# Kernel tuning notes

Measured on AMD Instinct MI355X. Metric: run time of the kernel, lower is better.

Reference implementation:

```python
import jax, jax.numpy as jnp
import numpy as np

D_MODEL = 1024
NUM_HEADS = 16
BATCH = 2
SEQ = 2048


def setup_inputs() -> dict:
    key = jax.random.key(0)
    ks = jax.random.split(key, 5)
    scale = 1.0 / np.sqrt(D_MODEL)
    x = jax.random.normal(ks[0], (BATCH, SEQ, D_MODEL), dtype=jnp.float32)
    Wq = jax.random.normal(ks[1], (D_MODEL, D_MODEL), dtype=jnp.float32) * scale
    Wk = jax.random.normal(ks[2], (D_MODEL, D_MODEL), dtype=jnp.float32) * scale
    Wv = jax.random.normal(ks[3], (D_MODEL, D_MODEL), dtype=jnp.float32) * scale
    Wo = jax.random.normal(ks[4], (D_MODEL, D_MODEL), dtype=jnp.float32) * scale
    return {"x": x, "Wq": Wq, "Wk": Wk, "Wv": Wv, "Wo": Wo}


def reference(x, Wq, Wk, Wv, Wo):
    b, s, d_model = x.shape
    h = NUM_HEADS
    d_head = d_model // h
    # projections (Linear with weight [out,in]: y = x @ W^T)
    def split_heads(y):
        return y.reshape(b, s, h, d_head).transpose(0, 2, 1, 3)  # b h s d
    q = split_heads(x @ Wq.T)
    k = split_heads(x @ Wk.T)
    v = split_heads(x @ Wv.T)
    # full (non-flash) attention, as in the original
    att = jnp.einsum('bhsd,bhtd->bhst', q, k) / jnp.sqrt(jnp.float32(d_head)).astype(x.dtype)
    att = jax.nn.softmax(att, axis=-1)
    out = jnp.einsum('bhst,bhtd->bhsd', att, v)
    out = out.transpose(0, 2, 1, 3).reshape(b, s, d_model)
    return out @ Wo.T
```

## Files before the change

kernel.cpp:

```cpp
#include <hip/hip_runtime.h>
#include <stdint.h>

typedef __bf16 bf16_t;
typedef __bf16 bf16x4 __attribute__((ext_vector_type(4)));
typedef __bf16 bf16x8 __attribute__((ext_vector_type(8)));
typedef float  f32x4  __attribute__((ext_vector_type(4)));
typedef float  f32x16 __attribute__((ext_vector_type(16)));

#define D_MODEL 1024
#define SEQ     2048
#define BATCH   2
#define NHEAD   16
#define DHEAD   64
#define NROWS   (BATCH*SEQ)
#define LDT     72
#define LDA     72

__device__ __forceinline__ void async_ld16(const bf16_t* g, bf16_t* l) {
    __builtin_amdgcn_global_load_lds(
        (const __attribute__((address_space(1))) uint32_t*)(uintptr_t)g,
        (__attribute__((address_space(3))) uint32_t*)(uintptr_t)l,
        16, 0, 0);
}

__device__ __forceinline__ bf16x8 cvt8(f32x4 lo, f32x4 hi) {
    bf16x8 o;
#pragma unroll
    for (int i = 0; i < 4; ++i) { o[i] = (bf16_t)lo[i]; o[4 + i] = (bf16_t)hi[i]; }
    return o;
}

__global__ void __launch_bounds__(256)
k_cvt(const float* __restrict__ w0, const float* __restrict__ w1,
      const float* __restrict__ w2, const float* __restrict__ w3,
      const float* __restrict__ x,
      bf16_t* __restrict__ o0, bf16_t* __restrict__ o1,
      bf16_t* __restrict__ o2, bf16_t* __restrict__ o3,
      bf16_t* __restrict__ ox)
{
    const int blk = blockIdx.x;
    const float* s; bf16_t* d; int bi;
    if (blk < 2048) { s = x; d = ox; bi = blk; }
    else {
        const int t = blk - 2048, sel = t >> 9; bi = t & 511;
        s = (sel == 0) ? w0 : (sel == 1) ? w1 : (sel == 2) ? w2 : w3;
        d = (sel == 0) ? o0 : (sel == 1) ? o1 : (sel == 2) ? o2 : o3;
    }
    const size_t i = ((size_t)bi * 256 + threadIdx.x) * 8;
    *(bf16x8*)(d + i) = cvt8(*(const f32x4*)(s + i), *(const f32x4*)(s + i + 4));
}

template <int OUT_MODE>
__device__ __forceinline__ void gemm128(bf16_t* __restrict__ smem,
                                        const bf16_t* __restrict__ X,
                                        const bf16_t* __restrict__ W,
                                        void* __restrict__ Yv,
                                        int m0, int n0, float oscale)
{
    bf16_t* lA = smem;
    bf16_t* lB = smem + 128 * 32;

    const int tid  = threadIdx.x;
    const int lane = tid & 63;
    const int w    = tid >> 6;
    const int l15  = lane & 15;
    const int quad = lane >> 4;

    const int c0 = tid, c1 = tid + 256;
    const int r0 = c0 >> 2, r1 = c1 >> 2;
    const int kc0 = (c0 & 3) ^ ((r0 >> 1) & 3);
    const int kc1 = (c1 & 3) ^ ((r1 >> 1) & 3);
    const bf16_t* gA0 = X + (size_t)(m0 + r0) * D_MODEL + kc0 * 8;
    const bf16_t* gA1 = X + (size_t)(m0 + r1) * D_MODEL + kc1 * 8;
    const bf16_t* gB0 = W + (size_t)(n0 + r0) * D_MODEL + kc0 * 8;
    const bf16_t* gB1 = W + (size_t)(n0 + r1) * D_MODEL + kc1 * 8;

    int am[4], bn[4];
    const int mw = (w >> 1) * 64, nw = (w & 1) * 64;
#pragma unroll
    for (int i = 0; i < 4; ++i) {
        const int ra = mw + i * 16 + l15;
        am[i] = ra * 32 + (quad ^ ((ra >> 1) & 3)) * 8;
        const int rb = nw + i * 16 + l15;
        bn[i] = rb * 32 + (quad ^ ((rb >> 1) & 3)) * 8;
    }

    f32x4 acc[4][4];
#pragma unroll
    for (int i = 0; i < 4; ++i)
#pragma unroll
        for (int j = 0; j < 4; ++j) acc[i][j] = f32x4{0.f, 0.f, 0.f, 0.f};

    for (int k0 = 0; k0 < D_MODEL; k0 += 32) {
        __syncthreads();
        async_ld16(gA0 + k0, &lA[c0 * 8]);
        async_ld16(gA1 + k0, &lA[c1 * 8]);
        async_ld16(gB0 + k0, &lB[c0 * 8]);
        async_ld16(gB1 + k0, &lB[c1 * 8]);
        __syncthreads();

        bf16x8 af[4], bfr[4];
#pragma unroll
        for (int i = 0; i < 4; ++i) af[i]  = *(const bf16x8*)&lA[am[i]];
#pragma unroll
        for (int i = 0; i < 4; ++i) bfr[i] = *(const bf16x8*)&lB[bn[i]];
#pragma unroll
        for (int mi = 0; mi < 4; ++mi)
#pragma unroll
            for (int ni = 0; ni < 4; ++ni)
                acc[mi][ni] = __builtin_amdgcn_mfma_f32_16x16x32_bf16(
                    af[mi], bfr[ni], acc[mi][ni], 0, 0, 0);
    }

    if constexpr (OUT_MODE == 1) {
        bf16_t* lT = smem;
#pragma unroll
        for (int h0 = 0; h0 < 2; ++h0) {
            __syncthreads();
            if ((w >> 1) == h0) {
#pragma unroll
                for (int mi = 0; mi < 4; ++mi)
#pragma unroll
                    for (int ni = 0; ni < 4; ++ni) {
                        bf16x4 pk;
#pragma unroll
                        for (int r = 0; r < 4; ++r)
                            pk[r] = (bf16_t)(acc[mi][ni][r] * oscale);
                        const int col = nw + ni * 16 + l15;
                        *(bf16x4*)&lT[col * LDT + mi * 16 + quad * 4] = pk;
                    }
            }
            __syncthreads();
            const int col = tid & 127;
            const int seg = tid >> 7;
            const int brow = m0 + h0 * 64;
            const int b = brow >> 11, sb = brow & 2047;
            const int cg = n0 + col;
            bf16_t* dst = (bf16_t*)Yv +
                ((size_t)((b << 4) | (cg >> 6)) * 64 + (cg & 63)) * SEQ + sb;
#pragma unroll
            for (int u = 0; u < 4; ++u)
                *(bf16x8*)(dst + seg * 32 + u * 8) =
                    *(const bf16x8*)&lT[col * LDT + seg * 32 + u * 8];
        }
    } else {
#pragma unroll
        for (int mi = 0; mi < 4; ++mi)
#pragma unroll
            for (int ni = 0; ni < 4; ++ni)
#pragma unroll
                for (int r = 0; r < 4; ++r) {
                    const int row = m0 + mw + mi * 16 + quad * 4 + r;
                    const int col = n0 + nw + ni * 16 + l15;
                    const float vv = acc[mi][ni][r] * oscale;
                    if constexpr (OUT_MODE == 0)
                        ((bf16_t*)Yv)[(size_t)row * D_MODEL + col] = (bf16_t)vv;
                    else
                        ((float*)Yv)[(size_t)row * D_MODEL + col] = vv;
                }
    }
}

__global__ void __launch_bounds__(256)
k_gemm_qkv(const bf16_t* __restrict__ X,
           const bf16_t* __restrict__ Wq, const bf16_t* __restrict__ Wk,
           const bf16_t* __restrict__ Wv,
           bf16_t* __restrict__ Qb, bf16_t* __restrict__ Kb, bf16_t* __restrict__ Vt)
{
    __shared__ __align__(16) bf16_t smem[128 * LDT];
    const int sel = blockIdx.y >> 3;
    const int n0  = (blockIdx.y & 7) * 128;
    const int m0  = blockIdx.x * 128;
    if (sel == 0)      gemm128<0>(smem, X, Wq, Qb, m0, n0, 0.125f);
    else if (sel == 1) gemm128<0>(smem, X, Wk, Kb, m0, n0, 1.0f);
    else               gemm128<1>(smem, X, Wv, Vt, m0, n0, 1.0f);
}

__global__ void __launch_bounds__(256)
k_gemm_out(const bf16_t* __restrict__ X, const bf16_t* __restrict__ W,
           float* __restrict__ Y)
{
    __shared__ __align__(16) bf16_t smem[128 * LDT];
    gemm128<2>(smem, X, W, Y, blockIdx.x * 128, blockIdx.y * 128, 1.0f);
}

__global__ void __launch_bounds__(256, 4)
k_attn(const bf16_t* __restrict__ Qb, const bf16_t* __restrict__ Kb,
       const bf16_t* __restrict__ Vt, bf16_t* __restrict__ Ob)
{
    __shared__ __align__(16) bf16_t lK[64 * LDA];
    __shared__ __align__(16) bf16_t lV[64 * LDA];
    __shared__ __align__(16) bf16_t Pm[64 * LDA];

    const int tid  = threadIdx.x;
    const int lane = tid & 63;
    const int w    = tid >> 6;
    const int l31  = lane & 31;
    const int h    = lane >> 5;
    const int a    = w & 1;
    const int b    = w >> 1;

    const int bh = blockIdx.x;
    const int b_ = bh >> 4, hh = bh & 15;
    const int q0 = blockIdx.y * 64;

    const size_t base = (size_t)b_ * SEQ * D_MODEL + (size_t)hh * DHEAD;
    const bf16_t* Qp = Qb + base;
    const bf16_t* Kp = Kb + base;
    const bf16_t* Vp = Vt + (size_t)bh * DHEAD * SEQ;

    const int qrow = q0 + b * 32 + l31;
    bf16x8 qf[4];
#pragma unroll
    for (int c = 0; c < 4; ++c)
        qf[c] = *(const bf16x8*)&Qp[(size_t)qrow * D_MODEL + c * 16 + h * 8];

    const int c0 = tid, c1 = tid + 256;
    const int r0 = c0 >> 3, ch0 = c0 & 7;
    const int r1 = c1 >> 3, ch1 = c1 & 7;
    const bf16_t* gK0 = Kp + (size_t)r0 * D_MODEL + ch0 * 8;
    const bf16_t* gK1 = Kp + (size_t)r1 * D_MODEL + ch1 * 8;
    const bf16_t* gV0 = Vp + (size_t)r0 * SEQ + ch0 * 8;
    const bf16_t* gV1 = Vp + (size_t)r1 * SEQ + ch1 * 8;
    const int sK0 = r0 * LDA + ch0 * 8, sK1 = r1 * LDA + ch1 * 8;

    bf16x8 ones;
#pragma unroll
    for (int i = 0; i < 8; ++i) ones[i] = (bf16_t)1.0f;

    f32x16 acc_o, acc_l;
#pragma unroll
    for (int i = 0; i < 16; ++i) { acc_o[i] = 0.f; acc_l[i] = 0.f; }

    bf16x8 pk0 = *(const bf16x8*)gK0;
    bf16x8 pk1 = *(const bf16x8*)gK1;
    bf16x8 pv0 = *(const bf16x8*)gV0;
    bf16x8 pv1 = *(const bf16x8*)gV1;

    for (int kv0 = 0; kv0 < SEQ; kv0 += 64) {
        __syncthreads();
        *(bf16x8*)&lK[sK0] = pk0;
        *(bf16x8*)&lK[sK1] = pk1;
        *(bf16x8*)&lV[sK0] = pv0;
        *(bf16x8*)&lV[sK1] = pv1;
        __syncthreads();

        const int nkv = kv0 + 64;
        if (nkv < SEQ) {
            pk0 = *(const bf16x8*)(gK0 + (size_t)nkv * D_MODEL);
            pk1 = *(const bf16x8*)(gK1 + (size_t)nkv * D_MODEL);
            pv0 = *(const bf16x8*)(gV0 + nkv);
            pv1 = *(const bf16x8*)(gV1 + nkv);
        }

        f32x16 st;
#pragma unroll
        for (int i = 0; i < 16; ++i) st[i] = 0.f;
#pragma unroll
        for (int c = 0; c < 4; ++c) {
            bf16x8 kf = *(const bf16x8*)&lK[(a * 32 + l31) * LDA + c * 16 + h * 8];
            st = __builtin_amdgcn_mfma_f32_32x32x16_bf16(kf, qf[c], st, 0, 0, 0);
        }

#pragma unroll
        for (int g = 0; g < 4; ++g) {
            bf16x4 pp;
#pragma unroll
            for (int r = 0; r < 4; ++r) pp[r] = (bf16_t)__expf(st[g * 4 + r]);
            *(bf16x4*)&Pm[(b * 32 + l31) * LDA + a * 32 + g * 8 + h * 4] = pp;
        }
        __syncthreads();

#pragma unroll
        for (int c = 0; c < 4; ++c) {
            bf16x8 pf = *(const bf16x8*)&Pm[(b * 32 + l31) * LDA + c * 16 + h * 8];
            bf16x8 vf = *(const bf16x8*)&lV[(a * 32 + l31) * LDA + c * 16 + h * 8];
            acc_l = __builtin_amdgcn_mfma_f32_32x32x16_bf16(pf, ones, acc_l, 0, 0, 0);
            acc_o = __builtin_amdgcn_mfma_f32_32x32x16_bf16(pf, vf, acc_o, 0, 0, 0);
        }
    }

#pragma unroll
    for (int g = 0; g < 4; ++g)
#pragma unroll
        for (int r = 0; r < 4; ++r) {
            const int ql  = r + 8 * g + 4 * h;
            const int row = b_ * SEQ + q0 + b * 32 + ql;
            const int col = hh * DHEAD + a * 32 + l31;
            Ob[(size_t)row * D_MODEL + col] =
                (bf16_t)(acc_o[g * 4 + r] / acc_l[g * 4 + r]);
        }
}

extern "C" void kernel_launch(void* const* d_in, const int* in_sizes, int n_in,
                              void* d_out, int out_size, void* d_ws, size_t ws_size,
                              hipStream_t stream)
{
    const float* x  = (const float*)d_in[0];
    const float* Wq = (const float*)d_in[1];
    const float* Wk = (const float*)d_in[2];
    const float* Wv = (const float*)d_in[3];
    const float* Wo = (const float*)d_in[4];
    float* out = (float*)d_out;

    const size_t wmat = (size_t)D_MODEL * D_MODEL;
    const size_t mat  = (size_t)NROWS * D_MODEL;
    bf16_t* Wqb = (bf16_t*)d_ws;
    bf16_t* Wkb = Wqb + wmat;
    bf16_t* Wvb = Wkb + wmat;
    bf16_t* Wob = Wvb + wmat;
    bf16_t* Xb  = Wob + wmat;
    bf16_t* Qb  = Xb + mat;
    bf16_t* Kb  = Qb + mat;
    bf16_t* Vt  = Kb + mat;
    bf16_t* Ab  = Qb;

    dim3 blk(256);
    k_cvt<<<dim3(4096), blk, 0, stream>>>(Wq, Wk, Wv, Wo, x, Wqb, Wkb, Wvb, Wob, Xb);
    k_gemm_qkv<<<dim3(32, 24), blk, 0, stream>>>(Xb, Wqb, Wkb, Wvb, Qb, Kb, Vt);
    k_attn<<<dim3(32, 32), blk, 0, stream>>>(Qb, Kb, Vt, Ab);
    k_gemm_out<<<dim3(32, 8), blk, 0, stream>>>(Ab, Wob, out);
}
```

Baseline: 198.2 us.

## Load attention K/V tiles directly into swizzled LDS with async global loads

```diff
diff --git a/kernel.cpp b/kernel.cpp
--- a/kernel.cpp
+++ b/kernel.cpp
@@ -14,7 +14,7 @@
 #define DHEAD   64
 #define NROWS   (BATCH*SEQ)
 #define LDT     72
-#define LDA     72
+#define LDP     72
 
 __device__ __forceinline__ void async_ld16(const bf16_t* g, bf16_t* l) {
     __builtin_amdgcn_global_load_lds(
@@ -188,9 +188,9 @@
 k_attn(const bf16_t* __restrict__ Qb, const bf16_t* __restrict__ Kb,
        const bf16_t* __restrict__ Vt, bf16_t* __restrict__ Ob)
 {
-    __shared__ __align__(16) bf16_t lK[64 * LDA];
-    __shared__ __align__(16) bf16_t lV[64 * LDA];
-    __shared__ __align__(16) bf16_t Pm[64 * LDA];
+    __shared__ __align__(16) bf16_t lK[64 * 64];
+    __shared__ __align__(16) bf16_t lV[64 * 64];
+    __shared__ __align__(16) bf16_t Pm[64 * LDP];
 
     const int tid  = threadIdx.x;
     const int lane = tid & 63;
@@ -216,13 +216,22 @@
         qf[c] = *(const bf16x8*)&Qp[(size_t)qrow * D_MODEL + c * 16 + h * 8];
 
     const int c0 = tid, c1 = tid + 256;
-    const int r0 = c0 >> 3, ch0 = c0 & 7;
-    const int r1 = c1 >> 3, ch1 = c1 & 7;
-    const bf16_t* gK0 = Kp + (size_t)r0 * D_MODEL + ch0 * 8;
-    const bf16_t* gK1 = Kp + (size_t)r1 * D_MODEL + ch1 * 8;
-    const bf16_t* gV0 = Vp + (size_t)r0 * SEQ + ch0 * 8;
-    const bf16_t* gV1 = Vp + (size_t)r1 * SEQ + ch1 * 8;
-    const int sK0 = r0 * LDA + ch0 * 8, sK1 = r1 * LDA + ch1 * 8;
+    const int r0 = c0 >> 3, g0 = (c0 & 7) ^ (r0 & 7);
+    const int r1 = c1 >> 3, g1 = (c1 & 7) ^ (r1 & 7);
+    const bf16_t* gK0 = Kp + (size_t)r0 * D_MODEL + g0 * 8;
+    const bf16_t* gK1 = Kp + (size_t)r1 * D_MODEL + g1 * 8;
+    const bf16_t* gV0 = Vp + (size_t)r0 * SEQ + g0 * 8;
+    const bf16_t* gV1 = Vp + (size_t)r1 * SEQ + g1 * 8;
+
+    const int frow = a * 32 + l31;
+    int koff[4], voff[4], poff[4];
+#pragma unroll
+    for (int c = 0; c < 4; ++c) {
+        const int ci = 2 * c + h;
+        koff[c] = frow * 64 + (ci ^ (frow & 7)) * 8;
+        voff[c] = frow * 64 + (ci ^ (frow & 7)) * 8;
+        poff[c] = (b * 32 + l31) * LDP + c * 16 + h * 8;
+    }
 
     bf16x8 ones;
 #pragma unroll
@@ -232,33 +241,20 @@
 #pragma unroll
     for (int i = 0; i < 16; ++i) { acc_o[i] = 0.f; acc_l[i] = 0.f; }
 
-    bf16x8 pk0 = *(const bf16x8*)gK0;
-    bf16x8 pk1 = *(const bf16x8*)gK1;
-    bf16x8 pv0 = *(const bf16x8*)gV0;
-    bf16x8 pv1 = *(const bf16x8*)gV1;
-
     for (int kv0 = 0; kv0 < SEQ; kv0 += 64) {
         __syncthreads();
-        *(bf16x8*)&lK[sK0] = pk0;
-        *(bf16x8*)&lK[sK1] = pk1;
-        *(bf16x8*)&lV[sK0] = pv0;
-        *(bf16x8*)&lV[sK1] = pv1;
-        __syncthreads();
-
-        const int nkv = kv0 + 64;
-        if (nkv < SEQ) {
-            pk0 = *(const bf16x8*)(gK0 + (size_t)nkv * D_MODEL);
-            pk1 = *(const bf16x8*)(gK1 + (size_t)nkv * D_MODEL);
-            pv0 = *(const bf16x8*)(gV0 + nkv);
-            pv1 = *(const bf16x8*)(gV1 + nkv);
-        }
+        async_ld16(gK0 + (size_t)kv0 * D_MODEL, &lK[c0 * 8]);
+        async_ld16(gK1 + (size_t)kv0 * D_MODEL, &lK[c1 * 8]);
+        async_ld16(gV0 + kv0, &lV[c0 * 8]);
+        async_ld16(gV1 + kv0, &lV[c1 * 8]);
+        __syncthreads();
 
         f32x16 st;
 #pragma unroll
         for (int i = 0; i < 16; ++i) st[i] = 0.f;
 #pragma unroll
         for (int c = 0; c < 4; ++c) {
-            bf16x8 kf = *(const bf16x8*)&lK[(a * 32 + l31) * LDA + c * 16 + h * 8];
+            bf16x8 kf = *(const bf16x8*)&lK[koff[c]];
             st = __builtin_amdgcn_mfma_f32_32x32x16_bf16(kf, qf[c], st, 0, 0, 0);
         }
 
@@ -267,14 +263,14 @@
             bf16x4 pp;
 #pragma unroll
             for (int r = 0; r < 4; ++r) pp[r] = (bf16_t)__expf(st[g * 4 + r]);
-            *(bf16x4*)&Pm[(b * 32 + l31) * LDA + a * 32 + g * 8 + h * 4] = pp;
+            *(bf16x4*)&Pm[(b * 32 + l31) * LDP + a * 32 + g * 8 + h * 4] = pp;
         }
         __syncthreads();
 
 #pragma unroll
         for (int c = 0; c < 4; ++c) {
-            bf16x8 pf = *(const bf16x8*)&Pm[(b * 32 + l31) * LDA + c * 16 + h * 8];
-            bf16x8 vf = *(const bf16x8*)&lV[(a * 32 + l31) * LDA + c * 16 + h * 8];
+            bf16x8 pf = *(const bf16x8*)&Pm[poff[c]];
+            bf16x8 vf = *(const bf16x8*)&lV[voff[c]];
             acc_l = __builtin_amdgcn_mfma_f32_32x32x16_bf16(pf, ones, acc_l, 0, 0, 0);
             acc_o = __builtin_amdgcn_mfma_f32_32x32x16_bf16(pf, vf, acc_o, 0, 0, 0);
         }
```

After: 194.0 us. 1.02x faster.
